# Kernel tuning notes

Measured on AMD Instinct MI355X. Metric: run time of the kernel, lower is better.

Reference implementation:

```python
import jax, jax.numpy as jnp
import numpy as np

BS, M, D, D_EM, K_RET = 32, 32768, 1024, 128, 32
EPS = 1e-12

def unit_normalize(x):
    return x / jnp.sqrt(jnp.sum(x * x, axis=-1, keepdims=True) + EPS)

def setup_inputs() -> dict:
    key = jax.random.key(0)
    ks = jax.random.split(key, 12)
    s = lambda fan_in: 1.0 / np.sqrt(fan_in)
    return {
        "x": jax.random.normal(ks[0], (BS, D), jnp.float32),
        "y_wm": jax.random.normal(ks[1], (BS, D), jnp.float32),
        "em_K": unit_normalize(jax.random.normal(ks[2], (BS, M, D_EM), jnp.float32)),
        "em_V": jax.random.normal(ks[3], (BS, M, D_EM), jnp.float32) * 0.01,
        "em_S": jax.random.uniform(ks[4], (BS, M), jnp.float32),  # all > 0 (active)
        "Wq_em_w": jax.random.normal(ks[5], (2 * D, D_EM), jnp.float32) * s(2 * D),
        "Wq_em_b": jnp.zeros((D_EM,), jnp.float32),
        "Wq_cross_w": jax.random.normal(ks[6], (D, D_EM), jnp.float32) * s(D),
        "Wq_cross_b": jnp.zeros((D_EM,), jnp.float32),
        "Wo_w": jax.random.normal(ks[7], (D_EM, D), jnp.float32) * s(D_EM),
        "Wo_b": jnp.zeros((D,), jnp.float32),
        "ln_g": jnp.ones((D_EM,), jnp.float32),
        "ln_b": jnp.zeros((D_EM,), jnp.float32),
        "ffn1_w": jax.random.normal(ks[8], (D_EM, 4 * D_EM), jnp.float32) * s(D_EM),
        "ffn1_b": jnp.zeros((4 * D_EM,), jnp.float32),
        "ffn2_w": jax.random.normal(ks[9], (4 * D_EM, D_EM), jnp.float32) * s(4 * D_EM),
        "ffn2_b": jnp.zeros((D_EM,), jnp.float32),
    }

def layernorm(x, g, b):
    mu = jnp.mean(x, axis=-1, keepdims=True)
    var = jnp.mean((x - mu) ** 2, axis=-1, keepdims=True)
    return (x - mu) * jax.lax.rsqrt(var + 1e-5) * g + b

def reference(x, y_wm, em_K, em_V, em_S, Wq_em_w, Wq_em_b, Wq_cross_w, Wq_cross_b,
              Wo_w, Wo_b, ln_g, ln_b, ffn1_w, ffn1_b, ffn2_w, ffn2_b):
    # query over concatenated (x, y_wm), unit-normalized
    q = unit_normalize(jnp.concatenate([x, y_wm], axis=-1) @ Wq_em_w + Wq_em_b)  # [BS, D_em]
    # masked cosine similarity scan over all M slots
    scores = jnp.einsum('bd,bmd->bm', q, em_K)                                   # [BS, M]
    scores = jnp.where(em_S > 0, scores, -jnp.inf)
    topk_scores, topk_idx = jax.lax.top_k(scores, K_RET)                         # [BS, k]
    V_top = jnp.take_along_axis(em_V, topk_idx[:, :, None], axis=1)              # [BS, k, D_em]
    # cross-attention read over retrieved slots
    q_cross = x @ Wq_cross_w + Wq_cross_b                                        # [BS, D_em]
    attn = jnp.einsum('bd,bkd->bk', q_cross, V_top) * (D_EM ** -0.5) + topk_scores
    attn = jnp.where(jnp.isneginf(topk_scores), -jnp.inf, attn)
    attn = jnp.nan_to_num(jax.nn.softmax(attn, axis=-1), nan=0.0)
    out = jnp.einsum('bk,bkd->bd', attn, V_top)                                  # [BS, D_em]
    # readout FFN (residual), exact GELU as in torch default
    h = layernorm(out, ln_g, ln_b)
    out = out + (jax.nn.gelu(h @ ffn1_w + ffn1_b, approximate=False) @ ffn2_w + ffn2_b)
    return out @ Wo_w + Wo_b                                                     # [BS, D]
```

## Files before the change

### kernel.cpp

```cpp
#include <hip/hip_runtime.h>
#include <math.h>

constexpr int kM  = 32768;
constexpr int kD  = 1024;
constexpr int kDE = 128;
constexpr int kK  = 32;
constexpr int kCap = 2048;
constexpr int kLBuf = 128;
constexpr float kT0 = 0.20f;

typedef float f4 __attribute__((ext_vector_type(4)));

__device__ __forceinline__ int score_bin(float s) {
  float w = (s + 1.0f) * 128.0f;
  w = fminf(fmaxf(w, 0.0f), 255.0f);
  return (int)w;
}
__device__ __forceinline__ unsigned long long pack_key(float s, int idx) {
  unsigned u = __float_as_uint(s);
  u = (u & 0x80000000u) ? ~u : (u | 0x80000000u);
  return ((unsigned long long)u << 32) | (unsigned)(~idx);
}

__global__ __launch_bounds__(1024) void qproj_kernel(
    const float* __restrict__ x, const float* __restrict__ y,
    const float* __restrict__ Wqe, const float* __restrict__ bqe,
    const float* __restrict__ Wqc, const float* __restrict__ bqc,
    float* __restrict__ q, float* __restrict__ qc,
    unsigned int* __restrict__ gcnt, unsigned int* __restrict__ gflag) {
  const int b = blockIdx.x, t = threadIdx.x;
  const int s = t >> 7, j = t & 127;

  if (t == 0) { gcnt[b] = 0u; gflag[b] = 0u; }

  const float* xb = x + b * kD;
  const float* yb = y + b * kD;

  const float* src1 = (s < 4) ? xb : yb;
  const int off1 = (s < 4) ? s * 256 : s * 256 - 1024;
  const int wb1 = s * 256;
  float a1[4] = {0.f, 0.f, 0.f, 0.f};
#pragma unroll 8
  for (int i0 = 0; i0 < 256; i0 += 4) {
#pragma unroll
    for (int u = 0; u < 4; ++u)
      a1[u] += src1[off1 + i0 + u] * Wqe[(wb1 + i0 + u) * kDE + j];
  }
  const int r2 = s * 128;
  float a2[4] = {0.f, 0.f, 0.f, 0.f};
#pragma unroll 8
  for (int i0 = 0; i0 < 128; i0 += 4) {
#pragma unroll
    for (int u = 0; u < 4; ++u)
      a2[u] += xb[r2 + i0 + u] * Wqc[(r2 + i0 + u) * kDE + j];
  }

  __shared__ float p1[8][128];
  __shared__ float p2[8][128];
  __shared__ float redn[2];
  p1[s][j] = (a1[0] + a1[1]) + (a1[2] + a1[3]);
  p2[s][j] = (a2[0] + a2[1]) + (a2[2] + a2[3]);
  __syncthreads();

  float a = 0.f, c = 0.f;
  if (t < 128) {
    a = bqe[t];
    c = bqc[t];
#pragma unroll
    for (int ss = 0; ss < 8; ++ss) { a += p1[ss][t]; c += p2[ss][t]; }
  }
  float sq = a * a;
#pragma unroll
  for (int m = 1; m < 64; m <<= 1) sq += __shfl_xor(sq, m);
  if (t == 0 || t == 64) redn[t >> 6] = sq;
  __syncthreads();
  if (t < 128) {
    const float inv = 1.f / sqrtf(redn[0] + redn[1] + 1e-12f);
    q[b * kDE + t] = a * inv;
    qc[b * kDE + t] = c;
  }
}

__global__ __launch_bounds__(256) void scores_kernel(
    const float* __restrict__ emK, const float* __restrict__ emS,
    const float* __restrict__ q, float* __restrict__ sc,
    unsigned int* __restrict__ gcnt, unsigned long long* __restrict__ gcand,
    unsigned int* __restrict__ gflag) {
  const int b = blockIdx.y, chunk = blockIdx.x;
  const int wave = threadIdx.x >> 6;
  const int lane = threadIdx.x & 63;
  const int half = lane >> 5;
  const int l32 = lane & 31;

  __shared__ unsigned int lcnt;
  __shared__ unsigned int lbase;
  __shared__ unsigned long long lbuf[kLBuf];
  if (threadIdx.x == 0) lcnt = 0u;
  __syncthreads();

  const float4 qf = *reinterpret_cast<const float4*>(q + b * kDE + l32 * 4);
  const int rowbase = chunk * 512 + wave * 128;
  const float* Kb = emK + (size_t)b * kM * kDE;
  const float* Sb = emS + (size_t)b * kM;
  float* scb = sc + (size_t)b * kM;

  for (int it = 0; it < 8; ++it) {
    const int A = rowbase + it * 16 + half * 8;
    const float* p = Kb + (size_t)A * kDE + l32 * 4;
    const f4 k0 = __builtin_nontemporal_load((const f4*)(p));
    const f4 k1 = __builtin_nontemporal_load((const f4*)(p + kDE));
    const f4 k2 = __builtin_nontemporal_load((const f4*)(p + 2 * kDE));
    const f4 k3 = __builtin_nontemporal_load((const f4*)(p + 3 * kDE));
    const f4 k4 = __builtin_nontemporal_load((const f4*)(p + 4 * kDE));
    const f4 k5 = __builtin_nontemporal_load((const f4*)(p + 5 * kDE));
    const f4 k6 = __builtin_nontemporal_load((const f4*)(p + 6 * kDE));
    const f4 k7 = __builtin_nontemporal_load((const f4*)(p + 7 * kDE));

    float d0 = fmaf(k0.w, qf.w, fmaf(k0.z, qf.z, fmaf(k0.y, qf.y, k0.x * qf.x)));
    float d1 = fmaf(k1.w, qf.w, fmaf(k1.z, qf.z, fmaf(k1.y, qf.y, k1.x * qf.x)));
    float d2 = fmaf(k2.w, qf.w, fmaf(k2.z, qf.z, fmaf(k2.y, qf.y, k2.x * qf.x)));
    float d3 = fmaf(k3.w, qf.w, fmaf(k3.z, qf.z, fmaf(k3.y, qf.y, k3.x * qf.x)));
    float d4 = fmaf(k4.w, qf.w, fmaf(k4.z, qf.z, fmaf(k4.y, qf.y, k4.x * qf.x)));
    float d5 = fmaf(k5.w, qf.w, fmaf(k5.z, qf.z, fmaf(k5.y, qf.y, k5.x * qf.x)));
    float d6 = fmaf(k6.w, qf.w, fmaf(k6.z, qf.z, fmaf(k6.y, qf.y, k6.x * qf.x)));
    float d7 = fmaf(k7.w, qf.w, fmaf(k7.z, qf.z, fmaf(k7.y, qf.y, k7.x * qf.x)));

#pragma unroll
    for (int m = 1; m < 32; m <<= 1) {
      d0 += __shfl_xor(d0, m);
      d1 += __shfl_xor(d1, m);
      d2 += __shfl_xor(d2, m);
      d3 += __shfl_xor(d3, m);
      d4 += __shfl_xor(d4, m);
      d5 += __shfl_xor(d5, m);
      d6 += __shfl_xor(d6, m);
      d7 += __shfl_xor(d7, m);
    }
    const float e0 = (l32 & 1) ? d1 : d0;
    const float e1 = (l32 & 1) ? d3 : d2;
    const float e2 = (l32 & 1) ? d5 : d4;
    const float e3 = (l32 & 1) ? d7 : d6;
    const float g0 = (l32 & 2) ? e1 : e0;
    const float g1 = (l32 & 2) ? e3 : e2;
    const float sel = (l32 & 4) ? g1 : g0;

    const float sv = Sb[A + (l32 & 7)];
    const float val = (sv > 0.f) ? sel : -INFINITY;
    if (l32 < 8) {
      const int row = A + l32;
      __builtin_nontemporal_store(val, &scb[row]);
      if (val >= kT0) {
        const unsigned pos = atomicAdd(&lcnt, 1u);
        if (pos < (unsigned)kLBuf) lbuf[pos] = pack_key(val, row);
      }
    }
  }
  __syncthreads();

  const unsigned c = min(lcnt, (unsigned)kLBuf);
  if (threadIdx.x == 0) {
    lbase = atomicAdd(&gcnt[b], c);
    if (lcnt > (unsigned)kLBuf) atomicOr(&gflag[b], 1u);
  }
  __syncthreads();
  const unsigned base = lbase;
  for (unsigned i = threadIdx.x; i < c; i += 256) {
    const unsigned pos = base + i;
    if (pos < (unsigned)kCap) gcand[(size_t)b * kCap + pos] = lbuf[i];
  }
}

__global__ __launch_bounds__(512) void finish_kernel(
    const float* __restrict__ sc, const unsigned int* __restrict__ gcnt,
    const unsigned long long* __restrict__ gcand,
    const unsigned int* __restrict__ gflag,
    const float* __restrict__ emV, const float* __restrict__ qc,
    const float* __restrict__ lng, const float* __restrict__ lnb,
    const float* __restrict__ f1w, const float* __restrict__ f1b,
    const float* __restrict__ f2w, const float* __restrict__ f2b,
    const float* __restrict__ Wo, const float* __restrict__ Wob,
    float* __restrict__ out) {
  const int b = blockIdx.x, t = threadIdx.x;
  const int wave = t >> 6, lane = t & 63;

  __shared__ unsigned long long ck[kCap];
  __shared__ int nS;
  __shared__ float outvS[32];
  __shared__ int outiS[32];
  __shared__ float Vt[32][128];
  __shared__ float qcl[128];
  __shared__ float wgt[32];
  __shared__ float hS[128];
  __shared__ float y1S[512];
  __shared__ float p2S[4][128];
  __shared__ float o2S[128];
  __shared__ float redA[2];
  __shared__ float redB[2];

  const unsigned cnt = gcnt[b];
  const unsigned flag = gflag[b];
  const float* scb = sc + (size_t)b * kM;
  if (t < 128) qcl[t] = qc[b * kDE + t];
  if (t < 32) { outvS[t] = -INFINITY; outiS[t] = 0; }

  if (flag == 0u && cnt >= 32u && cnt <= (unsigned)kCap) {
    for (unsigned i = t; i < cnt; i += 512)
      ck[i] = gcand[(size_t)b * kCap + i];
    if (t == 0) nS = (int)cnt;
  } else {
    __shared__ unsigned int shist[256];
    __shared__ int Bsh;
    __shared__ unsigned int cnt2;
    if (t < 256) shist[t] = 0u;
    if (t == 0) { Bsh = 0; cnt2 = 0u; }
    __syncthreads();
    for (int i = t; i < kM; i += 512)
      atomicAdd(&shist[score_bin(scb[i])], 1u);
    __syncthreads();
    for (int off = 1; off < 256; off <<= 1) {
      unsigned v = 0;
      if (t < 256) {
        v = shist[t];
        if (t + off < 256) v += shist[t + off];
      }
      __syncthreads();
      if (t < 256) shist[t] = v;
      __syncthreads();
    }
    if (t < 256 && shist[t] >= 32u) atomicMax(&Bsh, t);
    __syncthreads();
    const int B = Bsh;
    for (int i = t; i < kM; i += 512) {
      const float s = scb[i];
      if (score_bin(s) >= B) {
        const unsigned pos = atomicAdd(&cnt2, 1u);
        if (pos < (unsigned)kCap) ck[pos] = pack_key(s, i);
      }
    }
    __syncthreads();
    if (t == 0) nS = (int)min(cnt2, (unsigned)kCap);
  }
  __syncthreads();
  const int n = nS;

  unsigned long long mykey0 = 0, mykey1 = 0, mykey2 = 0, mykey3 = 0;
  if (t < n) mykey0 = ck[t];
  if (t + 512 < n) mykey1 = ck[t + 512];
  if (t + 1024 < n) mykey2 = ck[t + 1024];
  if (t + 1536 < n) mykey3 = ck[t + 1536];
  int r0 = 0, r1 = 0, r2 = 0, r3 = 0;
  for (int i = 0; i < n; ++i) {
    const unsigned long long o = ck[i];
    r0 += (o > mykey0);
    r1 += (o > mykey1);
    r2 += (o > mykey2);
    r3 += (o > mykey3);
  }
  auto emit = [&](unsigned long long key, int rank, int slot) {
    if (slot < n && rank < 32) {
      const unsigned mono = (unsigned)(key >> 32);
      const unsigned u = (mono & 0x80000000u) ? (mono & 0x7fffffffu) : ~mono;
      outvS[rank] = __uint_as_float(u);
      outiS[rank] = (int)(~(unsigned)key);
    }
  };
  emit(mykey0, r0, t);
  emit(mykey1, r1, t + 512);
  emit(mykey2, r2, t + 1024);
  emit(mykey3, r3, t + 1536);
  __syncthreads();

  const float* Vb = emV + (size_t)b * kM * kDE;
#pragma unroll
  for (int e = t; e < 32 * 128; e += 512) {
    const int r = e >> 7, ccol = e & 127;
    Vt[r][ccol] = Vb[(size_t)outiS[r] * kDE + ccol];
  }
  __syncthreads();

#pragma unroll
  for (int kk2 = 0; kk2 < 4; ++kk2) {
    const int k = wave * 4 + kk2;
    float p = Vt[k][2 * lane] * qcl[2 * lane] + Vt[k][2 * lane + 1] * qcl[2 * lane + 1];
#pragma unroll
    for (int m = 1; m < 64; m <<= 1) p += __shfl_xor(p, m);
    if (lane == 0) {
      const float tv = outvS[k];
      wgt[k] = (tv == -INFINITY) ? -INFINITY : fmaf(p, 0.08838834764831845f, tv);
    }
  }
  __syncthreads();

  if (t < 32) {
    const float lg = wgt[t];
    float mx = lg;
#pragma unroll
    for (int m = 1; m < 32; m <<= 1) mx = fmaxf(mx, __shfl_xor(mx, m));
    float e = (mx == -INFINITY || lg == -INFINITY) ? 0.f : __expf(lg - mx);
    float ssum = e;
#pragma unroll
    for (int m = 1; m < 32; m <<= 1) ssum += __shfl_xor(ssum, m);
    wgt[t] = (ssum > 0.f) ? e / ssum : 0.f;
  }
  __syncthreads();

  float od = 0.f;
  if (t < 128) {
#pragma unroll 8
    for (int k = 0; k < 32; ++k) od += wgt[k] * Vt[k][t];
  }
  float s1 = (t < 128) ? od : 0.f;
  float s2 = (t < 128) ? od * od : 0.f;
#pragma unroll
  for (int m = 1; m < 64; m <<= 1) {
    s1 += __shfl_xor(s1, m);
    s2 += __shfl_xor(s2, m);
  }
  if (lane == 0 && wave < 2) { redA[wave] = s1; redB[wave] = s2; }
  __syncthreads();
  const float sum1 = redA[0] + redA[1];
  const float sum2 = redB[0] + redB[1];
  const float mu = sum1 * (1.f / 128.f);
  const float var = sum2 * (1.f / 128.f) - mu * mu;
  const float rstd = 1.f / sqrtf(var + 1e-5f);
  if (t < 128) hS[t] = (od - mu) * rstd * lng[t] + lnb[t];
  __syncthreads();

  {
    float acc = f1b[t];
#pragma unroll 8
    for (int d = 0; d < 128; ++d) acc += hS[d] * f1w[(size_t)d * 512 + t];
    y1S[t] = 0.5f * acc * (1.f + erff(acc * 0.7071067811865476f));
  }
  __syncthreads();

  {
    const int g = t >> 7, ccol = t & 127;
    float acc = 0.f;
#pragma unroll 8
    for (int jj = 0; jj < 128; ++jj)
      acc += y1S[g * 128 + jj] * f2w[(size_t)(g * 128 + jj) * 128 + ccol];
    p2S[g][ccol] = acc;
  }
  __syncthreads();
  if (t < 128)
    o2S[t] = od + f2b[t] + ((p2S[0][t] + p2S[1][t]) + (p2S[2][t] + p2S[3][t]));
  __syncthreads();

  float acc0 = Wob[t], acc1 = Wob[t + 512];
#pragma unroll 8
  for (int d = 0; d < 128; ++d) {
    const float hv = o2S[d];
    acc0 += hv * Wo[(size_t)d * kD + t];
    acc1 += hv * Wo[(size_t)d * kD + t + 512];
  }
  out[(size_t)b * kD + t] = acc0;
  out[(size_t)b * kD + t + 512] = acc1;
}

extern "C" void kernel_launch(void* const* d_in, const int* in_sizes, int n_in,
                              void* d_out, int out_size, void* d_ws, size_t ws_size,
                              hipStream_t stream) {
  const float* x   = (const float*)d_in[0];
  const float* y   = (const float*)d_in[1];
  const float* emK = (const float*)d_in[2];
  const float* emV = (const float*)d_in[3];
  const float* emS = (const float*)d_in[4];
  const float* Wqe = (const float*)d_in[5];
  const float* bqe = (const float*)d_in[6];
  const float* Wqc = (const float*)d_in[7];
  const float* bqc = (const float*)d_in[8];
  const float* Wo  = (const float*)d_in[9];
  const float* Wob = (const float*)d_in[10];
  const float* lng = (const float*)d_in[11];
  const float* lnb = (const float*)d_in[12];
  const float* f1w = (const float*)d_in[13];
  const float* f1b = (const float*)d_in[14];
  const float* f2w = (const float*)d_in[15];
  const float* f2b = (const float*)d_in[16];
  float* out = (float*)d_out;

  float* ws = (float*)d_ws;
  float* q  = ws;
  float* qc = ws + 4096;
  float* sc = ws + 8192;
  unsigned int* gcnt  = (unsigned int*)(ws + 8192 + 32 * kM);
  unsigned int* gflag = gcnt + 32;
  unsigned long long* gcand =
      (unsigned long long*)(gcnt + 64);

  hipLaunchKernelGGL(qproj_kernel, dim3(32), dim3(1024), 0, stream,
                     x, y, Wqe, bqe, Wqc, bqc, q, qc, gcnt, gflag);
  hipLaunchKernelGGL(scores_kernel, dim3(64, 32), dim3(256), 0, stream,
                     emK, emS, q, sc, gcnt, gcand, gflag);
  hipLaunchKernelGGL(finish_kernel, dim3(32), dim3(512), 0, stream,
                     sc, gcnt, gcand, gflag, emV, qc, lng, lnb,
                     f1w, f1b, f2w, f2b, Wo, Wob, out);
}
```

Measured before the change: 157.6 us.

## Fuse query projection, scoring, and top-k finish into one persistent kernel with flags

Merges the three kernels into a single 1024-block launch. The query projection is split across 256 blocks that write partial sums. Scoring blocks spin on per-batch acquire/release flags, using generation counters, until their query is ready. The last-arriving chunk block for each batch (chunk 0) waits on completion flags and then runs the top-k selection and the FFN readout. This removes two launch boundaries and lets the projection work spread across more blocks, at the cost of cross-block spin-waits. Those waits depend on all 1024 blocks being co-resident (launch bounds 256,4), or the kernel risks deadlock.

```diff
diff --git a/kernel.cpp b/kernel.cpp
--- a/kernel.cpp
+++ b/kernel.cpp
@@ -5,8 +5,9 @@
 constexpr int kD  = 1024;
 constexpr int kDE = 128;
 constexpr int kK  = 32;
-constexpr int kCap = 2048;
-constexpr int kLBuf = 128;
+constexpr int kNB   = 1024;
+constexpr int kCap  = 2048;
+constexpr int kLBuf = 256;
 constexpr float kT0 = 0.20f;
 
 typedef float f4 __attribute__((ext_vector_type(4)));
@@ -21,272 +22,294 @@
   u = (u & 0x80000000u) ? ~u : (u | 0x80000000u);
   return ((unsigned long long)u << 32) | (unsigned)(~idx);
 }
-
-__global__ __launch_bounds__(1024) void qproj_kernel(
+__device__ __forceinline__ unsigned ld_acq(unsigned* p) {
+  return __hip_atomic_load(p, __ATOMIC_ACQUIRE, __HIP_MEMORY_SCOPE_AGENT);
+}
+__device__ __forceinline__ void st_rel(unsigned* p, unsigned v) {
+  __hip_atomic_store(p, v, __ATOMIC_RELEASE, __HIP_MEMORY_SCOPE_AGENT);
+}
+
+__global__ __launch_bounds__(256, 4) void fused_kernel(
     const float* __restrict__ x, const float* __restrict__ y,
+    const float* __restrict__ emK, const float* __restrict__ emV,
+    const float* __restrict__ emS,
     const float* __restrict__ Wqe, const float* __restrict__ bqe,
     const float* __restrict__ Wqc, const float* __restrict__ bqc,
-    float* __restrict__ q, float* __restrict__ qc,
-    unsigned int* __restrict__ gcnt, unsigned int* __restrict__ gflag) {
-  const int b = blockIdx.x, t = threadIdx.x;
-  const int s = t >> 7, j = t & 127;
-
-  if (t == 0) { gcnt[b] = 0u; gflag[b] = 0u; }
-
-  const float* xb = x + b * kD;
-  const float* yb = y + b * kD;
-
-  const float* src1 = (s < 4) ? xb : yb;
-  const int off1 = (s < 4) ? s * 256 : s * 256 - 1024;
-  const int wb1 = s * 256;
-  float a1[4] = {0.f, 0.f, 0.f, 0.f};
-#pragma unroll 8
-  for (int i0 = 0; i0 < 256; i0 += 4) {
-#pragma unroll
-    for (int u = 0; u < 4; ++u)
-      a1[u] += src1[off1 + i0 + u] * Wqe[(wb1 + i0 + u) * kDE + j];
-  }
-  const int r2 = s * 128;
-  float a2[4] = {0.f, 0.f, 0.f, 0.f};
-#pragma unroll 8
-  for (int i0 = 0; i0 < 128; i0 += 4) {
-#pragma unroll
-    for (int u = 0; u < 4; ++u)
-      a2[u] += xb[r2 + i0 + u] * Wqc[(r2 + i0 + u) * kDE + j];
-  }
-
-  __shared__ float p1[8][128];
-  __shared__ float p2[8][128];
-  __shared__ float redn[2];
-  p1[s][j] = (a1[0] + a1[1]) + (a1[2] + a1[3]);
-  p2[s][j] = (a2[0] + a2[1]) + (a2[2] + a2[3]);
-  __syncthreads();
-
-  float a = 0.f, c = 0.f;
-  if (t < 128) {
-    a = bqe[t];
-    c = bqc[t];
-#pragma unroll
-    for (int ss = 0; ss < 8; ++ss) { a += p1[ss][t]; c += p2[ss][t]; }
-  }
-  float sq = a * a;
-#pragma unroll
-  for (int m = 1; m < 64; m <<= 1) sq += __shfl_xor(sq, m);
-  if (t == 0 || t == 64) redn[t >> 6] = sq;
-  __syncthreads();
-  if (t < 128) {
-    const float inv = 1.f / sqrtf(redn[0] + redn[1] + 1e-12f);
-    q[b * kDE + t] = a * inv;
-    qc[b * kDE + t] = c;
-  }
-}
-
-__global__ __launch_bounds__(256) void scores_kernel(
-    const float* __restrict__ emK, const float* __restrict__ emS,
-    const float* __restrict__ q, float* __restrict__ sc,
-    unsigned int* __restrict__ gcnt, unsigned long long* __restrict__ gcand,
-    unsigned int* __restrict__ gflag) {
-  const int b = blockIdx.y, chunk = blockIdx.x;
-  const int wave = threadIdx.x >> 6;
-  const int lane = threadIdx.x & 63;
-  const int half = lane >> 5;
-  const int l32 = lane & 31;
-
-  __shared__ unsigned int lcnt;
-  __shared__ unsigned int lbase;
-  __shared__ unsigned long long lbuf[kLBuf];
-  if (threadIdx.x == 0) lcnt = 0u;
-  __syncthreads();
-
-  const float4 qf = *reinterpret_cast<const float4*>(q + b * kDE + l32 * 4);
-  const int rowbase = chunk * 512 + wave * 128;
-  const float* Kb = emK + (size_t)b * kM * kDE;
-  const float* Sb = emS + (size_t)b * kM;
-  float* scb = sc + (size_t)b * kM;
-
-  for (int it = 0; it < 8; ++it) {
-    const int A = rowbase + it * 16 + half * 8;
-    const float* p = Kb + (size_t)A * kDE + l32 * 4;
-    const f4 k0 = __builtin_nontemporal_load((const f4*)(p));
-    const f4 k1 = __builtin_nontemporal_load((const f4*)(p + kDE));
-    const f4 k2 = __builtin_nontemporal_load((const f4*)(p + 2 * kDE));
-    const f4 k3 = __builtin_nontemporal_load((const f4*)(p + 3 * kDE));
-    const f4 k4 = __builtin_nontemporal_load((const f4*)(p + 4 * kDE));
-    const f4 k5 = __builtin_nontemporal_load((const f4*)(p + 5 * kDE));
-    const f4 k6 = __builtin_nontemporal_load((const f4*)(p + 6 * kDE));
-    const f4 k7 = __builtin_nontemporal_load((const f4*)(p + 7 * kDE));
-
-    float d0 = fmaf(k0.w, qf.w, fmaf(k0.z, qf.z, fmaf(k0.y, qf.y, k0.x * qf.x)));
-    float d1 = fmaf(k1.w, qf.w, fmaf(k1.z, qf.z, fmaf(k1.y, qf.y, k1.x * qf.x)));
-    float d2 = fmaf(k2.w, qf.w, fmaf(k2.z, qf.z, fmaf(k2.y, qf.y, k2.x * qf.x)));
-    float d3 = fmaf(k3.w, qf.w, fmaf(k3.z, qf.z, fmaf(k3.y, qf.y, k3.x * qf.x)));
-    float d4 = fmaf(k4.w, qf.w, fmaf(k4.z, qf.z, fmaf(k4.y, qf.y, k4.x * qf.x)));
-    float d5 = fmaf(k5.w, qf.w, fmaf(k5.z, qf.z, fmaf(k5.y, qf.y, k5.x * qf.x)));
-    float d6 = fmaf(k6.w, qf.w, fmaf(k6.z, qf.z, fmaf(k6.y, qf.y, k6.x * qf.x)));
-    float d7 = fmaf(k7.w, qf.w, fmaf(k7.z, qf.z, fmaf(k7.y, qf.y, k7.x * qf.x)));
-
-#pragma unroll
-    for (int m = 1; m < 32; m <<= 1) {
-      d0 += __shfl_xor(d0, m);
-      d1 += __shfl_xor(d1, m);
-      d2 += __shfl_xor(d2, m);
-      d3 += __shfl_xor(d3, m);
-      d4 += __shfl_xor(d4, m);
-      d5 += __shfl_xor(d5, m);
-      d6 += __shfl_xor(d6, m);
-      d7 += __shfl_xor(d7, m);
-    }
-    const float e0 = (l32 & 1) ? d1 : d0;
-    const float e1 = (l32 & 1) ? d3 : d2;
-    const float e2 = (l32 & 1) ? d5 : d4;
-    const float e3 = (l32 & 1) ? d7 : d6;
-    const float g0 = (l32 & 2) ? e1 : e0;
-    const float g1 = (l32 & 2) ? e3 : e2;
-    const float sel = (l32 & 4) ? g1 : g0;
-
-    const float sv = Sb[A + (l32 & 7)];
-    const float val = (sv > 0.f) ? sel : -INFINITY;
-    if (l32 < 8) {
-      const int row = A + l32;
-      __builtin_nontemporal_store(val, &scb[row]);
-      if (val >= kT0) {
-        const unsigned pos = atomicAdd(&lcnt, 1u);
-        if (pos < (unsigned)kLBuf) lbuf[pos] = pack_key(val, row);
-      }
-    }
-  }
-  __syncthreads();
-
-  const unsigned c = min(lcnt, (unsigned)kLBuf);
-  if (threadIdx.x == 0) {
-    lbase = atomicAdd(&gcnt[b], c);
-    if (lcnt > (unsigned)kLBuf) atomicOr(&gflag[b], 1u);
-  }
-  __syncthreads();
-  const unsigned base = lbase;
-  for (unsigned i = threadIdx.x; i < c; i += 256) {
-    const unsigned pos = base + i;
-    if (pos < (unsigned)kCap) gcand[(size_t)b * kCap + pos] = lbuf[i];
-  }
-}
-
-__global__ __launch_bounds__(512) void finish_kernel(
-    const float* __restrict__ sc, const unsigned int* __restrict__ gcnt,
-    const unsigned long long* __restrict__ gcand,
-    const unsigned int* __restrict__ gflag,
-    const float* __restrict__ emV, const float* __restrict__ qc,
+    const float* __restrict__ Wo,  const float* __restrict__ Wob,
     const float* __restrict__ lng, const float* __restrict__ lnb,
     const float* __restrict__ f1w, const float* __restrict__ f1b,
     const float* __restrict__ f2w, const float* __restrict__ f2b,
-    const float* __restrict__ Wo, const float* __restrict__ Wob,
-    float* __restrict__ out) {
-  const int b = blockIdx.x, t = threadIdx.x;
+    float* __restrict__ out,
+    float* __restrict__ pq, float* __restrict__ pqc,
+    float* __restrict__ sc, unsigned long long* __restrict__ gcand,
+    unsigned* __restrict__ gcnt, unsigned* __restrict__ gflag,
+    unsigned* __restrict__ slot, unsigned* __restrict__ flagq,
+    unsigned* __restrict__ cflag) {
+  const int blk = blockIdx.x, t = threadIdx.x;
   const int wave = t >> 6, lane = t & 63;
 
-  __shared__ unsigned long long ck[kCap];
-  __shared__ int nS;
+  __shared__ unsigned genS;
+  __shared__ float ql[128];
+  __shared__ float redn2[2];
+  __shared__ unsigned lcnt, lbase;
+  __shared__ unsigned long long lbuf[kLBuf];
+  __shared__ float qcl[128];
+  __shared__ unsigned long long ck2[kCap];
+  __shared__ int nS2;
+  __shared__ unsigned shist[256];
+  __shared__ int Bsh;
+  __shared__ unsigned cnt2;
   __shared__ float outvS[32];
   __shared__ int outiS[32];
-  __shared__ float Vt[32][128];
-  __shared__ float qcl[128];
   __shared__ float wgt[32];
   __shared__ float hS[128];
   __shared__ float y1S[512];
-  __shared__ float p2S[4][128];
+  __shared__ float p2S[2][128];
   __shared__ float o2S[128];
-  __shared__ float redA[2];
-  __shared__ float redB[2];
-
-  const unsigned cnt = gcnt[b];
-  const unsigned flag = gflag[b];
+  __shared__ float redA[2], redB[2];
+
+  if (t == 0) {
+    const unsigned g = slot[blk] + 1u;
+    slot[blk] = g;
+    genS = g;
+  }
+  __syncthreads();
+  const unsigned gen = genS;
+
+  if (blk < 256) {
+    const int qb = blk >> 3, slice = blk & 7;
+    const int h = t >> 7, j = t & 127;
+    const int S = slice * 2 + h;
+    const float* srcA = (S < 8) ? (x + qb * kD + S * 128)
+                                : (y + qb * kD + (S - 8) * 128);
+    const float* wA = Wqe + (size_t)(S * 128) * kDE + j;
+    float s0 = 0.f, s1 = 0.f, s2 = 0.f, s3 = 0.f;
+#pragma unroll 8
+    for (int i = 0; i < 128; i += 4) {
+      s0 += srcA[i]     * wA[(size_t)(i)     * kDE];
+      s1 += srcA[i + 1] * wA[(size_t)(i + 1) * kDE];
+      s2 += srcA[i + 2] * wA[(size_t)(i + 2) * kDE];
+      s3 += srcA[i + 3] * wA[(size_t)(i + 3) * kDE];
+    }
+    pq[(qb * 16 + S) * 128 + j] = (s0 + s1) + (s2 + s3);
+
+    const float* srcB = x + qb * kD + S * 64;
+    const float* wB = Wqc + (size_t)(S * 64) * kDE + j;
+    float c0 = 0.f, c1 = 0.f, c2 = 0.f, c3 = 0.f;
+#pragma unroll 8
+    for (int i = 0; i < 64; i += 4) {
+      c0 += srcB[i]     * wB[(size_t)(i)     * kDE];
+      c1 += srcB[i + 1] * wB[(size_t)(i + 1) * kDE];
+      c2 += srcB[i + 2] * wB[(size_t)(i + 2) * kDE];
+      c3 += srcB[i + 3] * wB[(size_t)(i + 3) * kDE];
+    }
+    pqc[(qb * 16 + S) * 128 + j] = (c0 + c1) + (c2 + c3);
+
+    if (slice == 0 && t == 0) {
+      __hip_atomic_store(&gcnt[qb], 0u, __ATOMIC_RELAXED, __HIP_MEMORY_SCOPE_AGENT);
+      __hip_atomic_store(&gflag[qb], 0u, __ATOMIC_RELAXED, __HIP_MEMORY_SCOPE_AGENT);
+    }
+    __syncthreads();
+    if (t == 0) st_rel(&flagq[qb * 8 + slice], gen);
+  }
+
+  const int b = blk >> 5, chunk = blk & 31;
+
+  if (t < 8) {
+    while (ld_acq(&flagq[b * 8 + t]) != gen) __builtin_amdgcn_s_sleep(2);
+  }
+  if (t == 0) lcnt = 0u;
+  __syncthreads();
+
+  float aq = 0.f;
+  if (t < 128) {
+    aq = bqe[t];
+#pragma unroll
+    for (int S2 = 0; S2 < 16; ++S2) aq += pq[(b * 16 + S2) * 128 + t];
+    float sq = aq * aq;
+#pragma unroll
+    for (int m = 1; m < 64; m <<= 1) sq += __shfl_xor(sq, m);
+    if ((t & 63) == 0) redn2[t >> 6] = sq;
+  }
+  __syncthreads();
+  if (t < 128) ql[t] = aq * (1.f / sqrtf(redn2[0] + redn2[1] + 1e-12f));
+  __syncthreads();
+
+  {
+    const int half = lane >> 5, l32 = lane & 31;
+    const float4 qf = *reinterpret_cast<const float4*>(&ql[l32 * 4]);
+    const int rowbase = chunk * 1024 + wave * 256;
+    const float* Kb = emK + (size_t)b * kM * kDE;
+    const float* Sb = emS + (size_t)b * kM;
+    float* scb = sc + (size_t)b * kM;
+
+    for (int it = 0; it < 16; ++it) {
+      const int A = rowbase + it * 16 + half * 8;
+      const float* p = Kb + (size_t)A * kDE + l32 * 4;
+      const f4 k0 = __builtin_nontemporal_load((const f4*)(p));
+      const f4 k1 = __builtin_nontemporal_load((const f4*)(p + kDE));
+      const f4 k2 = __builtin_nontemporal_load((const f4*)(p + 2 * kDE));
+      const f4 k3 = __builtin_nontemporal_load((const f4*)(p + 3 * kDE));
+      const f4 k4 = __builtin_nontemporal_load((const f4*)(p + 4 * kDE));
+      const f4 k5 = __builtin_nontemporal_load((const f4*)(p + 5 * kDE));
+      const f4 k6 = __builtin_nontemporal_load((const f4*)(p + 6 * kDE));
+      const f4 k7 = __builtin_nontemporal_load((const f4*)(p + 7 * kDE));
+
+      float d0 = fmaf(k0.w, qf.w, fmaf(k0.z, qf.z, fmaf(k0.y, qf.y, k0.x * qf.x)));
+      float d1 = fmaf(k1.w, qf.w, fmaf(k1.z, qf.z, fmaf(k1.y, qf.y, k1.x * qf.x)));
+      float d2 = fmaf(k2.w, qf.w, fmaf(k2.z, qf.z, fmaf(k2.y, qf.y, k2.x * qf.x)));
+      float d3 = fmaf(k3.w, qf.w, fmaf(k3.z, qf.z, fmaf(k3.y, qf.y, k3.x * qf.x)));
+      float d4 = fmaf(k4.w, qf.w, fmaf(k4.z, qf.z, fmaf(k4.y, qf.y, k4.x * qf.x)));
+      float d5 = fmaf(k5.w, qf.w, fmaf(k5.z, qf.z, fmaf(k5.y, qf.y, k5.x * qf.x)));
+      float d6 = fmaf(k6.w, qf.w, fmaf(k6.z, qf.z, fmaf(k6.y, qf.y, k6.x * qf.x)));
+      float d7 = fmaf(k7.w, qf.w, fmaf(k7.z, qf.z, fmaf(k7.y, qf.y, k7.x * qf.x)));
+
+#pragma unroll
+      for (int m = 1; m < 32; m <<= 1) {
+        d0 += __shfl_xor(d0, m);
+        d1 += __shfl_xor(d1, m);
+        d2 += __shfl_xor(d2, m);
+        d3 += __shfl_xor(d3, m);
+        d4 += __shfl_xor(d4, m);
+        d5 += __shfl_xor(d5, m);
+        d6 += __shfl_xor(d6, m);
+        d7 += __shfl_xor(d7, m);
+      }
+      const float e0 = (l32 & 1) ? d1 : d0;
+      const float e1 = (l32 & 1) ? d3 : d2;
+      const float e2 = (l32 & 1) ? d5 : d4;
+      const float e3 = (l32 & 1) ? d7 : d6;
+      const float g0 = (l32 & 2) ? e1 : e0;
+      const float g1 = (l32 & 2) ? e3 : e2;
+      const float sel = (l32 & 4) ? g1 : g0;
+
+      const float sv = Sb[A + (l32 & 7)];
+      const float val = (sv > 0.f) ? sel : -INFINITY;
+      if (l32 < 8) {
+        const int row = A + l32;
+        __builtin_nontemporal_store(val, &scb[row]);
+        if (val >= kT0) {
+          const unsigned pos = atomicAdd(&lcnt, 1u);
+          if (pos < (unsigned)kLBuf) lbuf[pos] = pack_key(val, row);
+        }
+      }
+    }
+  }
+  __syncthreads();
+
+  const unsigned c = min(lcnt, (unsigned)kLBuf);
+  if (t == 0) {
+    lbase = atomicAdd(&gcnt[b], c);
+    if (lcnt > (unsigned)kLBuf) atomicOr(&gflag[b], 1u);
+  }
+  __syncthreads();
+  for (unsigned i = t; i < c; i += 256) {
+    const unsigned pos = lbase + i;
+    if (pos < (unsigned)kCap) gcand[(size_t)b * kCap + pos] = lbuf[i];
+  }
+  __syncthreads();
+  if (t == 0) st_rel(&cflag[b * 32 + chunk], gen);
+
+  if ((blk & 31) != 0) return;
+
+  if (t < 32) {
+    while (ld_acq(&cflag[b * 32 + t]) != gen) __builtin_amdgcn_s_sleep(2);
+  }
+  __syncthreads();
+
+  if (t < 128) {
+    float cc = bqc[t];
+#pragma unroll
+    for (int S2 = 0; S2 < 16; ++S2) cc += pqc[(b * 16 + S2) * 128 + t];
+    qcl[t] = cc;
+  }
+  if (t < 32) { outvS[t] = -INFINITY; outiS[t] = 0; }
+
+  const unsigned cnt = ld_acq(&gcnt[b]);
+  const unsigned flg = ld_acq(&gflag[b]);
   const float* scb = sc + (size_t)b * kM;
-  if (t < 128) qcl[t] = qc[b * kDE + t];
-  if (t < 32) { outvS[t] = -INFINITY; outiS[t] = 0; }
-
-  if (flag == 0u && cnt >= 32u && cnt <= (unsigned)kCap) {
-    for (unsigned i = t; i < cnt; i += 512)
-      ck[i] = gcand[(size_t)b * kCap + i];
-    if (t == 0) nS = (int)cnt;
+
+  if (flg == 0u && cnt >= 32u && cnt <= (unsigned)kCap) {
+    for (int i = t; i < kCap; i += 256)
+      ck2[i] = (i < (int)cnt) ? gcand[(size_t)b * kCap + i] : 0ull;
+    if (t == 0) nS2 = (int)cnt;
   } else {
-    __shared__ unsigned int shist[256];
-    __shared__ int Bsh;
-    __shared__ unsigned int cnt2;
-    if (t < 256) shist[t] = 0u;
+    shist[t] = 0u;
     if (t == 0) { Bsh = 0; cnt2 = 0u; }
     __syncthreads();
-    for (int i = t; i < kM; i += 512)
+    for (int i = t; i < kM; i += 256)
       atomicAdd(&shist[score_bin(scb[i])], 1u);
     __syncthreads();
     for (int off = 1; off < 256; off <<= 1) {
-      unsigned v = 0;
-      if (t < 256) {
-        v = shist[t];
-        if (t + off < 256) v += shist[t + off];
-      }
+      unsigned v = shist[t];
+      if (t + off < 256) v += shist[t + off];
       __syncthreads();
-      if (t < 256) shist[t] = v;
+      shist[t] = v;
       __syncthreads();
     }
-    if (t < 256 && shist[t] >= 32u) atomicMax(&Bsh, t);
+    if (shist[t] >= 32u) atomicMax(&Bsh, t);
     __syncthreads();
     const int B = Bsh;
-    for (int i = t; i < kM; i += 512) {
+    for (int i = t; i < kM; i += 256) {
       const float s = scb[i];
       if (score_bin(s) >= B) {
         const unsigned pos = atomicAdd(&cnt2, 1u);
-        if (pos < (unsigned)kCap) ck[pos] = pack_key(s, i);
+        if (pos < (unsigned)kCap) ck2[pos] = pack_key(s, i);
       }
     }
     __syncthreads();
-    if (t == 0) nS = (int)min(cnt2, (unsigned)kCap);
-  }
-  __syncthreads();
-  const int n = nS;
-
-  unsigned long long mykey0 = 0, mykey1 = 0, mykey2 = 0, mykey3 = 0;
-  if (t < n) mykey0 = ck[t];
-  if (t + 512 < n) mykey1 = ck[t + 512];
-  if (t + 1024 < n) mykey2 = ck[t + 1024];
-  if (t + 1536 < n) mykey3 = ck[t + 1536];
-  int r0 = 0, r1 = 0, r2 = 0, r3 = 0;
+    const int n0 = (int)min(cnt2, (unsigned)kCap);
+    for (int i = t; i < kCap; i += 256)
+      if (i >= n0) ck2[i] = 0ull;
+    if (t == 0) nS2 = n0;
+  }
+  __syncthreads();
+  const int n = nS2;
+
+  const unsigned long long K0 = ck2[t],        K1 = ck2[t + 256];
+  const unsigned long long K2 = ck2[t + 512],  K3 = ck2[t + 768];
+  const unsigned long long K4 = ck2[t + 1024], K5 = ck2[t + 1280];
+  const unsigned long long K6 = ck2[t + 1536], K7 = ck2[t + 1792];
+  int R0 = 0, R1 = 0, R2 = 0, R3 = 0, R4 = 0, R5 = 0, R6 = 0, R7 = 0;
   for (int i = 0; i < n; ++i) {
-    const unsigned long long o = ck[i];
-    r0 += (o > mykey0);
-    r1 += (o > mykey1);
-    r2 += (o > mykey2);
-    r3 += (o > mykey3);
-  }
-  auto emit = [&](unsigned long long key, int rank, int slot) {
-    if (slot < n && rank < 32) {
+    const unsigned long long o = ck2[i];
+    R0 += (o > K0); R1 += (o > K1); R2 += (o > K2); R3 += (o > K3);
+    R4 += (o > K4); R5 += (o > K5); R6 += (o > K6); R7 += (o > K7);
+  }
+  auto emit = [&](unsigned long long key, int rank, int slotI) {
+    if (slotI < n && rank < 32) {
       const unsigned mono = (unsigned)(key >> 32);
       const unsigned u = (mono & 0x80000000u) ? (mono & 0x7fffffffu) : ~mono;
       outvS[rank] = __uint_as_float(u);
       outiS[rank] = (int)(~(unsigned)key);
     }
   };
-  emit(mykey0, r0, t);
-  emit(mykey1, r1, t + 512);
-  emit(mykey2, r2, t + 1024);
-  emit(mykey3, r3, t + 1536);
+  emit(K0, R0, t);        emit(K1, R1, t + 256);
+  emit(K2, R2, t + 512);  emit(K3, R3, t + 768);
+  emit(K4, R4, t + 1024); emit(K5, R5, t + 1280);
+  emit(K6, R6, t + 1536); emit(K7, R7, t + 1792);
   __syncthreads();
 
   const float* Vb = emV + (size_t)b * kM * kDE;
-#pragma unroll
-  for (int e = t; e < 32 * 128; e += 512) {
-    const int r = e >> 7, ccol = e & 127;
-    Vt[r][ccol] = Vb[(size_t)outiS[r] * kDE + ccol];
-  }
-  __syncthreads();
-
-#pragma unroll
-  for (int kk2 = 0; kk2 < 4; ++kk2) {
-    const int k = wave * 4 + kk2;
-    float p = Vt[k][2 * lane] * qcl[2 * lane] + Vt[k][2 * lane + 1] * qcl[2 * lane + 1];
-#pragma unroll
-    for (int m = 1; m < 64; m <<= 1) p += __shfl_xor(p, m);
-    if (lane == 0) {
-      const float tv = outvS[k];
-      wgt[k] = (tv == -INFINITY) ? -INFINITY : fmaf(p, 0.08838834764831845f, tv);
+  {
+    const float qa = qcl[2 * lane], qb2 = qcl[2 * lane + 1];
+    float2 vv[8];
+    int ids[8];
+#pragma unroll
+    for (int kk = 0; kk < 8; ++kk) {
+      ids[kk] = outiS[wave * 8 + kk];
+      vv[kk] = *reinterpret_cast<const float2*>(&Vb[(size_t)ids[kk] * kDE + 2 * lane]);
+    }
+#pragma unroll
+    for (int kk = 0; kk < 8; ++kk) {
+      float p = vv[kk].x * qa + vv[kk].y * qb2;
+#pragma unroll
+      for (int m = 1; m < 64; m <<= 1) p += __shfl_xor(p, m);
+      if (lane == 0) {
+        const int k = wave * 8 + kk;
+        const float tv = outvS[k];
+        wgt[k] = (tv == -INFINITY) ? -INFINITY : fmaf(p, 0.08838834764831845f, tv);
+      }
     }
   }
   __syncthreads();
@@ -307,55 +330,61 @@
   float od = 0.f;
   if (t < 128) {
 #pragma unroll 8
-    for (int k = 0; k < 32; ++k) od += wgt[k] * Vt[k][t];
+    for (int k = 0; k < 32; ++k) od += wgt[k] * Vb[(size_t)outiS[k] * kDE + t];
   }
   float s1 = (t < 128) ? od : 0.f;
   float s2 = (t < 128) ? od * od : 0.f;
-#pragma unroll
-  for (int m = 1; m < 64; m <<= 1) {
-    s1 += __shfl_xor(s1, m);
-    s2 += __shfl_xor(s2, m);
-  }
-  if (lane == 0 && wave < 2) { redA[wave] = s1; redB[wave] = s2; }
-  __syncthreads();
-  const float sum1 = redA[0] + redA[1];
-  const float sum2 = redB[0] + redB[1];
-  const float mu = sum1 * (1.f / 128.f);
-  const float var = sum2 * (1.f / 128.f) - mu * mu;
+  if (t < 128) {
+#pragma unroll
+    for (int m = 1; m < 64; m <<= 1) {
+      s1 += __shfl_xor(s1, m);
+      s2 += __shfl_xor(s2, m);
+    }
+    if ((t & 63) == 0) { redA[t >> 6] = s1; redB[t >> 6] = s2; }
+  }
+  __syncthreads();
+  const float mu = (redA[0] + redA[1]) * (1.f / 128.f);
+  const float var = (redB[0] + redB[1]) * (1.f / 128.f) - mu * mu;
   const float rstd = 1.f / sqrtf(var + 1e-5f);
   if (t < 128) hS[t] = (od - mu) * rstd * lng[t] + lnb[t];
   __syncthreads();
 
+#pragma unroll
+  for (int jj = 0; jj < 2; ++jj) {
+    const int col = t + jj * 256;
+    float acc = f1b[col];
+#pragma unroll 8
+    for (int d = 0; d < 128; ++d) acc += hS[d] * f1w[(size_t)d * 512 + col];
+    y1S[col] = 0.5f * acc * (1.f + erff(acc * 0.7071067811865476f));
+  }
+  __syncthreads();
+
   {
-    float acc = f1b[t];
-#pragma unroll 8
-    for (int d = 0; d < 128; ++d) acc += hS[d] * f1w[(size_t)d * 512 + t];
-    y1S[t] = 0.5f * acc * (1.f + erff(acc * 0.7071067811865476f));
-  }
-  __syncthreads();
-
-  {
-    const int g = t >> 7, ccol = t & 127;
+    const int g = t >> 7, col = t & 127;
     float acc = 0.f;
 #pragma unroll 8
-    for (int jj = 0; jj < 128; ++jj)
-      acc += y1S[g * 128 + jj] * f2w[(size_t)(g * 128 + jj) * 128 + ccol];
-    p2S[g][ccol] = acc;
-  }
-  __syncthreads();
-  if (t < 128)
-    o2S[t] = od + f2b[t] + ((p2S[0][t] + p2S[1][t]) + (p2S[2][t] + p2S[3][t]));
-  __syncthreads();
-
-  float acc0 = Wob[t], acc1 = Wob[t + 512];
-#pragma unroll 8
+    for (int jj = 0; jj < 256; ++jj)
+      acc += y1S[g * 256 + jj] * f2w[(size_t)(g * 256 + jj) * 128 + col];
+    p2S[g][col] = acc;
+  }
+  __syncthreads();
+  if (t < 128) o2S[t] = od + f2b[t] + p2S[0][t] + p2S[1][t];
+  __syncthreads();
+
+  float a0 = Wob[t], a1 = Wob[t + 256], a2 = Wob[t + 512], a3 = Wob[t + 768];
+#pragma unroll 4
   for (int d = 0; d < 128; ++d) {
     const float hv = o2S[d];
-    acc0 += hv * Wo[(size_t)d * kD + t];
-    acc1 += hv * Wo[(size_t)d * kD + t + 512];
-  }
-  out[(size_t)b * kD + t] = acc0;
-  out[(size_t)b * kD + t + 512] = acc1;
+    a0 += hv * Wo[(size_t)d * kD + t];
+    a1 += hv * Wo[(size_t)d * kD + t + 256];
+    a2 += hv * Wo[(size_t)d * kD + t + 512];
+    a3 += hv * Wo[(size_t)d * kD + t + 768];
+  }
+  float* ob = out + (size_t)b * kD;
+  ob[t] = a0;
+  ob[t + 256] = a1;
+  ob[t + 512] = a2;
+  ob[t + 768] = a3;
 }
 
 extern "C" void kernel_launch(void* const* d_in, const int* in_sizes, int n_in,
@@ -381,19 +410,19 @@
   float* out = (float*)d_out;
 
   float* ws = (float*)d_ws;
-  float* q  = ws;
-  float* qc = ws + 4096;
-  float* sc = ws + 8192;
-  unsigned int* gcnt  = (unsigned int*)(ws + 8192 + 32 * kM);
-  unsigned int* gflag = gcnt + 32;
+  float* pq  = ws;
+  float* pqc = ws + 65536;
+  float* sc  = ws + 131072;
   unsigned long long* gcand =
-      (unsigned long long*)(gcnt + 64);
-
-  hipLaunchKernelGGL(qproj_kernel, dim3(32), dim3(1024), 0, stream,
-                     x, y, Wqe, bqe, Wqc, bqc, q, qc, gcnt, gflag);
-  hipLaunchKernelGGL(scores_kernel, dim3(64, 32), dim3(256), 0, stream,
-                     emK, emS, q, sc, gcnt, gcand, gflag);
-  hipLaunchKernelGGL(finish_kernel, dim3(32), dim3(512), 0, stream,
-                     sc, gcnt, gcand, gflag, emV, qc, lng, lnb,
-                     f1w, f1b, f2w, f2b, Wo, Wob, out);
-}
+      (unsigned long long*)(ws + 1179648);
+  unsigned* gcnt  = (unsigned*)(ws + 1310720);
+  unsigned* gflag = gcnt + 32;
+  unsigned* slot  = gflag + 32;
+  unsigned* flagq = slot + 1024;
+  unsigned* cflag = flagq + 256;
+
+  hipLaunchKernelGGL(fused_kernel, dim3(kNB), dim3(256), 0, stream,
+                     x, y, emK, emV, emS, Wqe, bqe, Wqc, bqc, Wo, Wob,
+                     lng, lnb, f1w, f1b, f2w, f2b, out,
+                     pq, pqc, sc, gcand, gcnt, gflag, slot, flagq, cflag);
+}
```

Result: slower. 286.8 us (+82.0%).
